# Performance work log

Hardware: AMD Instinct MI355X
Metric: run time of the kernel (lower is better)

## Reference

```python
import jax, jax.numpy as jnp
import numpy as np

HEADS = 3


def layernorm(x, scale, bias):
    mu = x.mean(-1, keepdims=True)
    var = ((x - mu) ** 2).mean(-1, keepdims=True)
    return (x - mu) * jax.lax.rsqrt(var + 1e-5) * scale + bias


def setup_inputs() -> dict:
    key = jax.random.key(0)
    ks = jax.random.split(key, 16)
    B, C, H, W = 8, 64, 32, 32
    hid, out, L = 384, 128, 3
    f32 = jnp.float32
    rn = lambda i, shape, sc: jax.random.normal(ks[i], shape, f32) * sc
    inp = {
        "x": rn(0, (B, C, H, W), 1.0),
        "W_enc": rn(1, (C, hid), 1.0 / np.sqrt(C)),
        "b_enc": jnp.zeros((hid,), f32),
        "gcn_W": rn(2, (L, hid, hid), 1.0 / np.sqrt(hid)),
        "gcn_b": jnp.zeros((L, hid), f32),
        "Wq": rn(3, (L, hid, hid), 1.0 / np.sqrt(hid)),
        "bq": jnp.zeros((L, hid), f32),
        "Wk": rn(4, (L, hid, hid), 1.0 / np.sqrt(hid)),
        "bk": jnp.zeros((L, hid), f32),
        "Wv": rn(5, (L, hid, hid), 1.0 / np.sqrt(hid)),
        "bv": jnp.zeros((L, hid), f32),
        "Wo": rn(6, (L, hid, hid), 1.0 / np.sqrt(hid)),
        "bo": jnp.zeros((L, hid), f32),
        "ln_scale": jnp.ones((L, 3, hid), f32),
        "ln_bias": jnp.zeros((L, 3, hid), f32),
        "mlp_W1": rn(7, (L, hid, 2 * hid), 1.0 / np.sqrt(hid)),
        "mlp_b1": jnp.zeros((L, 2 * hid), f32),
        "mlp_W2": rn(8, (L, 2 * hid, hid), 1.0 / np.sqrt(2 * hid)),
        "mlp_b2": jnp.zeros((L, hid), f32),
        "lin1_W": rn(9, (hid, hid), 1.0 / np.sqrt(hid)),
        "lin1_b": jnp.zeros((hid,), f32),
        "lin2_W": rn(10, (hid, out), 1.0 / np.sqrt(hid)),
        "lin2_b": jnp.zeros((out,), f32),
        "k": 16,
    }
    return inp


def reference(x, W_enc, b_enc, gcn_W, gcn_b, Wq, bq, Wk, bk, Wv, bv, Wo, bo,
              ln_scale, ln_bias, mlp_W1, mlp_b1, mlp_W2, mlp_b2,
              lin1_W, lin1_b, lin2_W, lin2_b, k):
    B, C, H, W = x.shape
    N = H * W
    L = gcn_W.shape[0]

    # node encoder (RWSE expand_x modeled as linear projection of pixel features)
    feats = x.reshape(B, C, N).transpose(0, 2, 1)            # [B, N, C]
    h0 = feats @ W_enc + b_enc                               # [B, N, hid]

    # cosine-similarity graph + kNN hypergraph build
    nh = h0 / jnp.linalg.norm(h0, axis=-1, keepdims=True)
    sim = jnp.einsum('bnd,bmd->bnm', nh, nh)                 # [B, N, N]
    sim = sim - 2.0 * jnp.eye(N, dtype=sim.dtype)            # exclude self-matches
    _, knn_idx = jax.lax.top_k(sim, k)                       # [B, N, k] neighbor (src) ids
    dst = jnp.broadcast_to(jnp.arange(N)[:, None], (N, k)).reshape(-1)  # [N*k]

    def gps_per_graph(hb, src_idx):
        src = src_idx.reshape(-1)                            # [N*k]
        deg = jax.ops.segment_sum(jnp.ones((N * k,), hb.dtype), dst, N) + 1.0  # self-loops
        norm = jax.lax.rsqrt(deg[src] * deg[dst])            # GCN sym norm
        hcur = hb
        for l in range(L):
            # --- local GCN message passing ---
            xw = hcur @ gcn_W[l] + gcn_b[l]                  # [N, hid]
            agg = jax.ops.segment_sum(xw[src] * norm[:, None], dst, N)
            agg = agg + xw / deg[:, None]                    # self-loop term
            h_local = layernorm(hcur + agg, ln_scale[l, 0], ln_bias[l, 0])
            # --- global multihead attention ---
            q = (hcur @ Wq[l] + bq[l]).reshape(N, HEADS, -1)
            kk = (hcur @ Wk[l] + bk[l]).reshape(N, HEADS, -1)
            v = (hcur @ Wv[l] + bv[l]).reshape(N, HEADS, -1)
            dh = q.shape[-1]
            scores = jnp.einsum('nhd,mhd->hnm', q, kk) * (1.0 / np.sqrt(dh))
            attn = jax.nn.softmax(scores, axis=-1)
            o = jnp.einsum('hnm,mhd->nhd', attn, v).reshape(N, -1) @ Wo[l] + bo[l]
            h_attn = layernorm(hcur + o, ln_scale[l, 1], ln_bias[l, 1])
            # --- combine + FFN ---
            out = h_local + h_attn
            out = out + jax.nn.relu(out @ mlp_W1[l] + mlp_b1[l]) @ mlp_W2[l] + mlp_b2[l]
            hcur = layernorm(out, ln_scale[l, 2], ln_bias[l, 2])
        return hcur.mean(axis=0)                             # global mean pool -> [hid]

    pooled = jax.vmap(gps_per_graph)(h0, knn_idx)            # [B, hid]
    z = jax.nn.relu(pooled @ lin1_W + lin1_b)
    return z @ lin2_W + lin2_b                               # [B, out]
```

## Files before the change

kernel.cpp:

```cpp
#include <hip/hip_runtime.h>
#include <hip/hip_bf16.h>

#define B_    8
#define C_    64
#define N_    1024
#define HID   384
#define OUTD  128
#define L_    3
#define KNN   16
#define NHEADS 3
#define DH    128

typedef __attribute__((ext_vector_type(8))) short    s16x8;
typedef __attribute__((ext_vector_type(4))) float    f32x4;
typedef __attribute__((ext_vector_type(8))) unsigned short u16x8;
typedef __attribute__((ext_vector_type(4))) unsigned short u16x4;

__device__ __forceinline__ ushort f2b(float f) {
    uint x = __float_as_uint(f);
    return (ushort)((x + 0x7fff + ((x >> 16) & 1)) >> 16);
}
__device__ __forceinline__ float b2f(uint u) {
    return __uint_as_float(u << 16);
}

__global__ void k_encode(const float* __restrict__ x, const float* __restrict__ Wenc,
                         const float* __restrict__ benc, float* __restrict__ h,
                         float* __restrict__ nh) {
    int bn = blockIdx.x;
    int b = bn >> 10;
    const float* xb = x + (long)b * C_ * N_ + (bn & 1023);
    int tid = threadIdx.x;
    __shared__ float red[128];
    float val[3];
    #pragma unroll
    for (int i = 0; i < 3; ++i) {
        int c0 = tid + i * 128;
        float acc = benc[c0];
        for (int c = 0; c < C_; ++c)
            acc += xb[c * N_] * Wenc[c * HID + c0];
        h[(long)bn * HID + c0] = acc;
        val[i] = acc;
    }
    float ss = 0.f;
    #pragma unroll
    for (int i = 0; i < 3; ++i) ss += val[i] * val[i];
    red[tid] = ss; __syncthreads();
    for (int s = 64; s > 0; s >>= 1) { if (tid < s) red[tid] += red[tid+s]; __syncthreads(); }
    float inv = 1.0f / sqrtf(red[0]);
    #pragma unroll
    for (int i = 0; i < 3; ++i)
        nh[(long)bn * HID + tid + i * 128] = val[i] * inv;
}

template<bool BT, bool RELU>
__global__ __launch_bounds__(256) void k_gemm(
        const float* __restrict__ A, const float* __restrict__ Bm,
        const float* __restrict__ bias, const float* __restrict__ resid,
        float* __restrict__ C, int M, int N, int K,
        long strideA, long strideB, long strideC) {
    __shared__ float As[16][68];
    __shared__ float Bs[16][68];
    int bz = blockIdx.z;
    A  += (long)bz * strideA;
    Bm += (long)bz * strideB;
    C  += (long)bz * strideC;
    int bm = blockIdx.y * 64, bn = blockIdx.x * 64;
    int tid = threadIdx.x;
    int ty = tid >> 4, tx = tid & 15;
    int lm = tid >> 2, lq = tid & 3;
    float acc[4][4] = {};
    for (int k0 = 0; k0 < K; k0 += 16) {
        {
            float4 av = *(const float4*)&A[(long)(bm + lm) * K + k0 + lq * 4];
            As[lq*4+0][lm] = av.x; As[lq*4+1][lm] = av.y;
            As[lq*4+2][lm] = av.z; As[lq*4+3][lm] = av.w;
        }
        if (BT) {
            float4 bv = *(const float4*)&Bm[(long)(bn + lm) * K + k0 + lq * 4];
            Bs[lq*4+0][lm] = bv.x; Bs[lq*4+1][lm] = bv.y;
            Bs[lq*4+2][lm] = bv.z; Bs[lq*4+3][lm] = bv.w;
        } else {
            int kk = tid >> 4, nq = tid & 15;
            float4 bv = *(const float4*)&Bm[(long)(k0 + kk) * N + bn + nq * 4];
            Bs[kk][nq*4+0] = bv.x; Bs[kk][nq*4+1] = bv.y;
            Bs[kk][nq*4+2] = bv.z; Bs[kk][nq*4+3] = bv.w;
        }
        __syncthreads();
        #pragma unroll
        for (int kk = 0; kk < 16; ++kk) {
            float4 a = *(const float4*)&As[kk][ty * 4];
            float4 b = *(const float4*)&Bs[kk][tx * 4];
            acc[0][0] += a.x*b.x; acc[0][1] += a.x*b.y; acc[0][2] += a.x*b.z; acc[0][3] += a.x*b.w;
            acc[1][0] += a.y*b.x; acc[1][1] += a.y*b.y; acc[1][2] += a.y*b.z; acc[1][3] += a.y*b.w;
            acc[2][0] += a.z*b.x; acc[2][1] += a.z*b.y; acc[2][2] += a.z*b.z; acc[2][3] += a.z*b.w;
            acc[3][0] += a.w*b.x; acc[3][1] += a.w*b.y; acc[3][2] += a.w*b.z; acc[3][3] += a.w*b.w;
        }
        __syncthreads();
    }
    #pragma unroll
    for (int i = 0; i < 4; ++i) {
        int row = bm + ty * 4 + i;
        #pragma unroll
        for (int j = 0; j < 4; ++j) {
            int col = bn + tx * 4 + j;
            float c = acc[i][j];
            if (bias)  c += bias[col];
            if (resid) c += resid[(long)row * N + col];
            if (RELU)  c = fmaxf(c, 0.f);
            C[(long)row * N + col] = c;
        }
    }
}

__global__ __launch_bounds__(256) void k_topk(const float* __restrict__ sim, int* __restrict__ knn) {
    int tid = threadIdx.x;
    int wave = tid >> 6, ll = tid & 63;
    int bn = blockIdx.x * 4 + wave;
    int b = bn >> 10, n = bn & 1023;
    const float* row = sim + (long)b * N_ * N_ + (long)n * N_;
    float v[16];
    #pragma unroll
    for (int j = 0; j < 16; ++j) {
        int m = ll + j * 64;
        v[j] = row[m] - (m == n ? 2.0f : 0.0f);
    }
    int* kout = knn + (long)bn * KNN;
    for (int it = 0; it < KNN; ++it) {
        float bv = v[0]; int bi = ll;
        #pragma unroll
        for (int j = 1; j < 16; ++j)
            if (v[j] > bv) { bv = v[j]; bi = ll + j * 64; }
        #pragma unroll
        for (int mask = 1; mask < 64; mask <<= 1) {
            float ov = __shfl_xor(bv, mask);
            int   oi = __shfl_xor(bi, mask);
            if (ov > bv || (ov == bv && oi < bi)) { bv = ov; bi = oi; }
        }
        if (ll == 0) kout[it] = bi;
        if ((bi & 63) == ll) v[bi >> 6] = -1e30f;
    }
}

__global__ void k_cast15(const float* __restrict__ g, const float* __restrict__ q,
                         const float* __restrict__ k, const float* __restrict__ v,
                         const float* __restrict__ o, ushort* __restrict__ out) {
    int z = blockIdx.z; int type = z / 3, l = z % 3;
    const float* in = (type == 0 ? g : type == 1 ? q : type == 2 ? k : type == 3 ? v : o)
                      + (long)l * HID * HID;
    ushort* op = out + (long)z * HID * HID;
    __shared__ float t[32][33];
    int c0 = blockIdx.x * 32, r0 = blockIdx.y * 32;
    int tid = threadIdx.x; int i = tid & 31, j4 = tid >> 5;
    #pragma unroll
    for (int rr = 0; rr < 4; ++rr) {
        int r = j4 * 4 + rr;
        t[r][i] = in[(long)(r0 + r) * HID + c0 + i];
    }
    __syncthreads();
    #pragma unroll
    for (int rr = 0; rr < 4; ++rr) {
        int c = j4 * 4 + rr;
        op[(long)(c0 + c) * HID + r0 + i] = f2b(t[i][c]);
    }
}

__global__ void k_castT(const float* __restrict__ in_, ushort* __restrict__ out_,
                        int R, int C) {
    long mz = (long)blockIdx.z * R * C;
    const float* in = in_ + mz;
    ushort* op = out_ + mz;
    __shared__ float t[32][33];
    int c0 = blockIdx.x * 32, r0 = blockIdx.y * 32;
    int tid = threadIdx.x; int i = tid & 31, j4 = tid >> 5;
    #pragma unroll
    for (int rr = 0; rr < 4; ++rr) {
        int r = j4 * 4 + rr;
        t[r][i] = in[(long)(r0 + r) * C + c0 + i];
    }
    __syncthreads();
    #pragma unroll
    for (int rr = 0; rr < 4; ++rr) {
        int c = j4 * 4 + rr;
        op[(long)(c0 + c) * R + r0 + i] = f2b(t[i][c]);
    }
}

__global__ __launch_bounds__(256) void k_castb(const float* __restrict__ in,
                                               ushort* __restrict__ out) {
    long i0 = ((long)blockIdx.x * 256 + threadIdx.x) * 8;
    float4 a0 = *(const float4*)&in[i0];
    float4 a1 = *(const float4*)&in[i0 + 4];
    u16x8 v;
    v[0]=f2b(a0.x); v[1]=f2b(a0.y); v[2]=f2b(a0.z); v[3]=f2b(a0.w);
    v[4]=f2b(a1.x); v[5]=f2b(a1.y); v[6]=f2b(a1.z); v[7]=f2b(a1.w);
    *(u16x8*)&out[i0] = v;
}

template<int OUTMODE, bool RELU>
__global__ __launch_bounds__(256) void k_mgemm(
        const ushort* __restrict__ A, const ushort* __restrict__ Wt,
        const float* __restrict__ bias, const float* __restrict__ resid,
        void* __restrict__ Cout, int M, int N, int K, long ldcT) {
    __shared__ ushort Al[128][40];
    __shared__ ushort Bl[128][40];
    int bm = blockIdx.y * 128, bnn = blockIdx.x * 128;
    int tid = threadIdx.x;
    int w = tid >> 6, l = tid & 63;
    int wm = w >> 1, wn = w & 1;
    int sr = tid >> 2, skq = (tid & 3) * 8;
    f32x4 acc[4][4] = {};
    for (int k0 = 0; k0 < K; k0 += 32) {
        *(u16x8*)&Al[sr][skq]      = *(const u16x8*)&A [(long)(bm + sr) * K + k0 + skq];
        *(u16x8*)&Al[sr + 64][skq] = *(const u16x8*)&A [(long)(bm + sr + 64) * K + k0 + skq];
        *(u16x8*)&Bl[sr][skq]      = *(const u16x8*)&Wt[(long)(bnn + sr) * K + k0 + skq];
        *(u16x8*)&Bl[sr + 64][skq] = *(const u16x8*)&Wt[(long)(bnn + sr + 64) * K + k0 + skq];
        __syncthreads();
        s16x8 af[4], bf[4];
        #pragma unroll
        for (int mi = 0; mi < 4; ++mi)
            af[mi] = *(const s16x8*)&Al[wm * 64 + mi * 16 + (l & 15)][(l >> 4) * 8];
        #pragma unroll
        for (int ni = 0; ni < 4; ++ni)
            bf[ni] = *(const s16x8*)&Bl[wn * 64 + ni * 16 + (l & 15)][(l >> 4) * 8];
        #pragma unroll
        for (int mi = 0; mi < 4; ++mi)
            #pragma unroll
            for (int ni = 0; ni < 4; ++ni)
                acc[mi][ni] = __builtin_amdgcn_mfma_f32_16x16x32_bf16(af[mi], bf[ni], acc[mi][ni], 0, 0, 0);
        __syncthreads();
    }
    #pragma unroll
    for (int mi = 0; mi < 4; ++mi) {
        int row0 = bm + wm * 64 + mi * 16 + (l >> 4) * 4;
        #pragma unroll
        for (int ni = 0; ni < 4; ++ni) {
            int coln = bnn + wn * 64 + ni * 16 + (l & 15);
            float bv = bias[coln];
            if (OUTMODE == 2) {
                u16x4 pk;
                #pragma unroll
                for (int reg = 0; reg < 4; ++reg)
                    pk[reg] = f2b(acc[mi][ni][reg] + bv);
                *(u16x4*)((ushort*)Cout + (long)coln * ldcT + row0) = pk;
            } else {
                #pragma unroll
                for (int reg = 0; reg < 4; ++reg) {
                    int rowg = row0 + reg;
                    float v = acc[mi][ni][reg] + bv;
                    if (resid) v += resid[(long)rowg * N + coln];
                    if (RELU)  v = fmaxf(v, 0.f);
                    if (OUTMODE == 0) ((float*)Cout)[(long)rowg * N + coln] = v;
                    else              ((ushort*)Cout)[(long)rowg * N + coln] = f2b(v);
                }
            }
        }
    }
}

__global__ void k_gcn_ln(const float* __restrict__ h, const float* __restrict__ xw,
                         const int* __restrict__ knn,
                         const float* __restrict__ lns, const float* __restrict__ lnb,
                         float* __restrict__ hlocal) {
    int bn = blockIdx.x; int b = bn >> 10;
    __shared__ int nb[KNN];
    __shared__ float red[128];
    int tid = threadIdx.x;
    if (tid < KNN) nb[tid] = knn[(long)bn * KNN + tid];
    __syncthreads();
    float val[3]; float sum = 0.f, ssq = 0.f;
    #pragma unroll
    for (int i = 0; i < 3; ++i) {
        int c = tid + i * 128;
        float acc = xw[(long)bn * HID + c];
        #pragma unroll
        for (int j = 0; j < KNN; ++j)
            acc += xw[((long)(b << 10) + nb[j]) * HID + c];
        float v = h[(long)bn * HID + c] + acc * (1.0f / 17.0f);
        val[i] = v; sum += v; ssq += v * v;
    }
    red[tid] = sum; __syncthreads();
    for (int s = 64; s > 0; s >>= 1) { if (tid < s) red[tid] += red[tid+s]; __syncthreads(); }
    sum = red[0]; __syncthreads();
    red[tid] = ssq; __syncthreads();
    for (int s = 64; s > 0; s >>= 1) { if (tid < s) red[tid] += red[tid+s]; __syncthreads(); }
    ssq = red[0];
    float mu = sum / HID;
    float var = ssq / HID - mu * mu;
    float inv = rsqrtf(var + 1e-5f);
    #pragma unroll
    for (int i = 0; i < 3; ++i) {
        int c = tid + i * 128;
        hlocal[(long)bn * HID + c] = (val[i] - mu) * inv * lns[c] + lnb[c];
    }
}

__global__ void k_addln(const float* __restrict__ a, const float* __restrict__ badd,
                        const float* __restrict__ post,
                        const float* __restrict__ lns, const float* __restrict__ lnb,
                        float* __restrict__ outp, ushort* __restrict__ bfout) {
    int bn = blockIdx.x;
    __shared__ float red[128];
    int tid = threadIdx.x;
    float val[3]; float sum = 0.f, ssq = 0.f;
    #pragma unroll
    for (int i = 0; i < 3; ++i) {
        int c = tid + i * 128;
        float v = a[(long)bn * HID + c];
        if (badd) v += badd[(long)bn * HID + c];
        val[i] = v; sum += v; ssq += v * v;
    }
    red[tid] = sum; __syncthreads();
    for (int s = 64; s > 0; s >>= 1) { if (tid < s) red[tid] += red[tid+s]; __syncthreads(); }
    sum = red[0]; __syncthreads();
    red[tid] = ssq; __syncthreads();
    for (int s = 64; s > 0; s >>= 1) { if (tid < s) red[tid] += red[tid+s]; __syncthreads(); }
    ssq = red[0];
    float mu = sum / HID;
    float var = ssq / HID - mu * mu;
    float inv = rsqrtf(var + 1e-5f);
    #pragma unroll
    for (int i = 0; i < 3; ++i) {
        int c = tid + i * 128;
        float o = (val[i] - mu) * inv * lns[c] + lnb[c];
        if (post) o += post[(long)bn * HID + c];
        outp[(long)bn * HID + c] = o;
        if (bfout) bfout[(long)bn * HID + c] = f2b(o);
    }
}

__global__ __launch_bounds__(256) void k_attn(const ushort* __restrict__ qb,
                                              const ushort* __restrict__ kb,
                                              const ushort* __restrict__ vt,
                                              ushort* __restrict__ o) {
    int b = blockIdx.z, hh = blockIdx.y, r0 = blockIdx.x * 16;
    __shared__ ushort sc[16][1032];
    __shared__ ushort kvt[9216];
    __shared__ float rowinv[16];
    int tid = threadIdx.x;
    int w = tid >> 6, l = tid & 63;
    s16x8 aq[4];
    const ushort* qrow = qb + ((long)(b * N_) + r0 + (l & 15)) * HID + hh * DH + (l >> 4) * 8;
    #pragma unroll
    for (int ks = 0; ks < 4; ++ks) aq[ks] = *(const s16x8*)(qrow + ks * 32);
    const float scale = 0.08838834764831845f;
    for (int m0 = 0; m0 < N_; m0 += 64) {
        {
            int key = tid >> 2, seg = tid & 3;
            const ushort* src = kb + ((long)(b * N_) + m0 + key) * HID + hh * DH + seg * 32;
            ushort* dst = &kvt[key * 136 + seg * 32];
            #pragma unroll
            for (int i = 0; i < 4; ++i)
                *(u16x8*)(dst + i * 8) = *(const u16x8*)(src + i * 8);
        }
        __syncthreads();
        f32x4 acc = {0.f, 0.f, 0.f, 0.f};
        #pragma unroll
        for (int ks = 0; ks < 4; ++ks) {
            s16x8 bk = *(const s16x8*)&kvt[(w * 16 + (l & 15)) * 136 + ks * 32 + (l >> 4) * 8];
            acc = __builtin_amdgcn_mfma_f32_16x16x32_bf16(aq[ks], bk, acc, 0, 0, 0);
        }
        int key = m0 + w * 16 + (l & 15);
        #pragma unroll
        for (int reg = 0; reg < 4; ++reg)
            sc[(l >> 4) * 4 + reg][key] = f2b(acc[reg] * scale);
        __syncthreads();
    }
    {
        int g = tid >> 5, l2 = tid & 31;
        #pragma unroll
        for (int rr = 0; rr < 2; ++rr) {
            int row = g + rr * 8;
            float v[32];
            #pragma unroll
            for (int i = 0; i < 16; ++i) {
                uint u = *(const uint*)&sc[row][l2 * 2 + i * 64];
                v[2*i]   = b2f(u & 0xffffu);
                v[2*i+1] = b2f(u >> 16);
            }
            float mx = v[0];
            #pragma unroll
            for (int i = 1; i < 32; ++i) mx = fmaxf(mx, v[i]);
            #pragma unroll
            for (int m = 16; m >= 1; m >>= 1) mx = fmaxf(mx, __shfl_xor(mx, m));
            float sm = 0.f;
            #pragma unroll
            for (int i = 0; i < 16; ++i) {
                float e0 = __expf(v[2*i]   - mx);
                float e1 = __expf(v[2*i+1] - mx);
                sm += e0 + e1;
                *(uint*)&sc[row][l2 * 2 + i * 64] = (uint)f2b(e0) | ((uint)f2b(e1) << 16);
            }
            #pragma unroll
            for (int m = 16; m >= 1; m >>= 1) sm += __shfl_xor(sm, m);
            if (l2 == 0) rowinv[row] = 1.0f / sm;
        }
    }
    __syncthreads();
    f32x4 zero = {0.f, 0.f, 0.f, 0.f};
    f32x4 oacc[2] = {zero, zero};
    for (int m0 = 0; m0 < N_; m0 += 64) {
        {
            int dim = tid >> 1, half = tid & 1;
            const ushort* src = vt + ((long)(hh * DH + dim)) * (B_ * N_) + b * N_ + m0 + half * 32;
            ushort* dst = &kvt[dim * 72 + half * 32];
            #pragma unroll
            for (int i = 0; i < 4; ++i)
                *(u16x8*)(dst + i * 8) = *(const u16x8*)(src + i * 8);
        }
        __syncthreads();
        #pragma unroll
        for (int ks = 0; ks < 2; ++ks) {
            s16x8 pf = *(const s16x8*)&sc[l & 15][m0 + ks * 32 + (l >> 4) * 8];
            #pragma unroll
            for (int d = 0; d < 2; ++d) {
                s16x8 vf = *(const s16x8*)&kvt[((w * 2 + d) * 16 + (l & 15)) * 72 + ks * 32 + (l >> 4) * 8];
                oacc[d] = __builtin_amdgcn_mfma_f32_16x16x32_bf16(pf, vf, oacc[d], 0, 0, 0);
            }
        }
        __syncthreads();
    }
    #pragma unroll
    for (int d = 0; d < 2; ++d) {
        int dim = (w * 2 + d) * 16 + (l & 15);
        #pragma unroll
        for (int reg = 0; reg < 4; ++reg) {
            int row = (l >> 4) * 4 + reg;
            o[((long)(b * N_) + r0 + row) * HID + hh * DH + dim] = f2b(oacc[d][reg] * rowinv[row]);
        }
    }
}

__global__ __launch_bounds__(384) void k_pool1(const float* __restrict__ h,
                                               float* __restrict__ partial) {
    int s = blockIdx.x, b = blockIdx.y;
    int c = threadIdx.x;
    const float* hp = h + ((long)(b * N_) + s * 32) * HID + c;
    float acc = 0.f;
    #pragma unroll
    for (int n = 0; n < 32; ++n) acc += hp[(long)n * HID];
    partial[((long)(b * 32) + s) * HID + c] = acc;
}
__global__ __launch_bounds__(384) void k_pool2(const float* __restrict__ partial,
                                               float* __restrict__ pooled) {
    int b = blockIdx.x;
    int c = threadIdx.x;
    const float* pp = partial + (long)(b * 32) * HID + c;
    float acc = 0.f;
    #pragma unroll
    for (int s = 0; s < 32; ++s) acc += pp[(long)s * HID];
    pooled[b * HID + c] = acc * (1.0f / N_);
}

__global__ void k_head(const float* __restrict__ pooled,
                       const float* __restrict__ w1, const float* __restrict__ b1,
                       const float* __restrict__ w2, const float* __restrict__ b2,
                       float* __restrict__ out) {
    int b = blockIdx.x; int tid = threadIdx.x;
    __shared__ float z[HID];
    float acc = b1[tid];
    for (int c = 0; c < HID; ++c) acc += pooled[b * HID + c] * w1[c * HID + tid];
    z[tid] = fmaxf(acc, 0.f);
    __syncthreads();
    if (tid < OUTD) {
        float a2 = b2[tid];
        for (int j = 0; j < HID; ++j) a2 += z[j] * w2[j * OUTD + tid];
        out[b * OUTD + tid] = a2;
    }
}

extern "C" void kernel_launch(void* const* d_in, const int* in_sizes, int n_in,
                              void* d_out, int out_size, void* d_ws, size_t ws_size,
                              hipStream_t stream) {
    const float* x       = (const float*)d_in[0];
    const float* W_enc   = (const float*)d_in[1];
    const float* b_enc   = (const float*)d_in[2];
    const float* gcn_W   = (const float*)d_in[3];
    const float* gcn_b   = (const float*)d_in[4];
    const float* Wq      = (const float*)d_in[5];
    const float* bq      = (const float*)d_in[6];
    const float* Wk      = (const float*)d_in[7];
    const float* bk      = (const float*)d_in[8];
    const float* Wv      = (const float*)d_in[9];
    const float* bv      = (const float*)d_in[10];
    const float* Wo      = (const float*)d_in[11];
    const float* bo      = (const float*)d_in[12];
    const float* ln_s    = (const float*)d_in[13];
    const float* ln_b    = (const float*)d_in[14];
    const float* mlp_W1  = (const float*)d_in[15];
    const float* mlp_b1  = (const float*)d_in[16];
    const float* mlp_W2  = (const float*)d_in[17];
    const float* mlp_b2  = (const float*)d_in[18];
    const float* lin1_W  = (const float*)d_in[19];
    const float* lin1_b  = (const float*)d_in[20];
    const float* lin2_W  = (const float*)d_in[21];
    const float* lin2_b  = (const float*)d_in[22];

    const long S = (long)B_ * N_ * HID;
    char* base = (char*)d_ws;
    float* h      = (float*)(base);
    float* tmp1   = (float*)(base + (size_t)S * 4);
    float* hlocal = (float*)(base + (size_t)S * 8);
    float* outb   = (float*)(base + (size_t)S * 12);
    char*  tzone  = base + (size_t)S * 16;
    float* proj   = (float*)(base + (size_t)S * 24);
    float*  sim = (float*)tzone;
    ushort* qbf = (ushort*)tzone;
    ushort* kbf = (ushort*)(tzone + (size_t)S * 2);
    ushort* vbT = (ushort*)(tzone + (size_t)S * 4);
    ushort* outb_bf = (ushort*)(tzone + (size_t)S * 6);
    ushort* tb  = (ushort*)tzone;
    int*    knn    = (int*)(base + (size_t)S * 28);
    float*  pooled = (float*)(base + (size_t)S * 28 + 524288);
    ushort* wts    = (ushort*)(base + (size_t)S * 28 + 524288 + 16384);
    const long SQ = (long)HID * HID;
    ushort* w1T = wts + 15 * SQ;
    ushort* w2T = w1T + 3 * (long)HID * 2 * HID;
    ushort* hb  = (ushort*)(base + (size_t)S * 28 + 524288 + 16384 + 7962624);
    float* partial = tmp1;
    ushort* obf = (ushort*)tmp1;

    k_cast15<<<dim3(12, 12, 15), 256, 0, stream>>>(gcn_W, Wq, Wk, Wv, Wo, wts);
    k_castT<<<dim3(24, 12, 3), 256, 0, stream>>>(mlp_W1, w1T, HID, 2 * HID);
    k_castT<<<dim3(12, 24, 3), 256, 0, stream>>>(mlp_W2, w2T, 2 * HID, HID);

    k_encode<<<B_ * N_, 128, 0, stream>>>(x, W_enc, b_enc, h, tmp1);
    k_gemm<true, false><<<dim3(16, 16, B_), 256, 0, stream>>>(
        tmp1, tmp1, nullptr, nullptr, sim, N_, N_, HID,
        (long)N_ * HID, (long)N_ * HID, (long)N_ * N_);
    k_topk<<<B_ * N_ / 4, 256, 0, stream>>>(sim, knn);
    k_castb<<<(int)(S / 2048), 256, 0, stream>>>(h, hb);

    const int M = B_ * N_;
    for (int l = 0; l < L_; ++l) {
        const ushort* gWt = wts + (long)(0 + l) * SQ;
        const ushort* wqT = wts + (long)(3 + l) * SQ;
        const ushort* wkT = wts + (long)(6 + l) * SQ;
        const ushort* wvT = wts + (long)(9 + l) * SQ;
        const ushort* woT = wts + (long)(12 + l) * SQ;
        const ushort* w1Tl = w1T + (long)l * HID * 2 * HID;
        const ushort* w2Tl = w2T + (long)l * HID * 2 * HID;
        const float* gB  = gcn_b + (long)l * HID;
        const float* bql = bq + (long)l * HID;
        const float* bkl = bk + (long)l * HID;
        const float* bvl = bv + (long)l * HID;
        const float* bol = bo + (long)l * HID;
        const float* b1l = mlp_b1 + (long)l * 2 * HID;
        const float* b2l = mlp_b2 + (long)l * HID;
        const float* ls0 = ln_s + (long)(l * 3 + 0) * HID; const float* lb0 = ln_b + (long)(l * 3 + 0) * HID;
        const float* ls1 = ln_s + (long)(l * 3 + 1) * HID; const float* lb1 = ln_b + (long)(l * 3 + 1) * HID;
        const float* ls2 = ln_s + (long)(l * 3 + 2) * HID; const float* lb2 = ln_b + (long)(l * 3 + 2) * HID;

        k_mgemm<0, false><<<dim3(HID / 128, M / 128), 256, 0, stream>>>(
            hb, gWt, gB, nullptr, tmp1, M, HID, HID, 0);
        k_gcn_ln<<<B_ * N_, 128, 0, stream>>>(h, tmp1, knn, ls0, lb0, hlocal);
        k_mgemm<1, false><<<dim3(HID / 128, M / 128), 256, 0, stream>>>(
            hb, wqT, bql, nullptr, qbf, M, HID, HID, 0);
        k_mgemm<1, false><<<dim3(HID / 128, M / 128), 256, 0, stream>>>(
            hb, wkT, bkl, nullptr, kbf, M, HID, HID, 0);
        k_mgemm<2, false><<<dim3(HID / 128, M / 128), 256, 0, stream>>>(
            hb, wvT, bvl, nullptr, vbT, M, HID, HID, (long)M);
        k_attn<<<dim3(N_ / 16, NHEADS, B_), 256, 0, stream>>>(qbf, kbf, vbT, obf);
        k_mgemm<0, false><<<dim3(HID / 128, M / 128), 256, 0, stream>>>(
            obf, woT, bol, nullptr, proj, M, HID, HID, 0);
        k_addln<<<B_ * N_, 128, 0, stream>>>(h, proj, hlocal, ls1, lb1, outb, outb_bf);
        k_mgemm<1, true><<<dim3(2 * HID / 128, M / 128), 256, 0, stream>>>(
            outb_bf, w1Tl, b1l, nullptr, tb, M, 2 * HID, HID, 0);
        k_mgemm<0, false><<<dim3(HID / 128, M / 128), 256, 0, stream>>>(
            tb, w2Tl, b2l, outb, tmp1, M, HID, 2 * HID, 0);
        k_addln<<<B_ * N_, 128, 0, stream>>>(tmp1, nullptr, nullptr, ls2, lb2, h, hb);
    }

    k_pool1<<<dim3(32, B_), 384, 0, stream>>>(h, partial);
    k_pool2<<<B_, 384, 0, stream>>>(partial, pooled);
    k_head<<<B_, HID, 0, stream>>>(pooled, lin1_W, lin1_b, lin2_W, lin2_b,
                                   (float*)d_out);
}
```

Baseline: 996.8 us.

## Use split-bf16 MFMA for similarity GEMM and fuse QKV projections

Measured after the change: 875.0 us. 1.14x faster.

```diff
diff --git a/kernel.cpp b/kernel.cpp
--- a/kernel.cpp
+++ b/kernel.cpp
@@ -26,7 +26,8 @@
 
 __global__ void k_encode(const float* __restrict__ x, const float* __restrict__ Wenc,
                          const float* __restrict__ benc, float* __restrict__ h,
-                         float* __restrict__ nh) {
+                         ushort* __restrict__ hb,
+                         ushort* __restrict__ nhh, ushort* __restrict__ nhl) {
     int bn = blockIdx.x;
     int b = bn >> 10;
     const float* xb = x + (long)b * C_ * N_ + (bn & 1023);
@@ -40,6 +41,7 @@
         for (int c = 0; c < C_; ++c)
             acc += xb[c * N_] * Wenc[c * HID + c0];
         h[(long)bn * HID + c0] = acc;
+        hb[(long)bn * HID + c0] = f2b(acc);
         val[i] = acc;
     }
     float ss = 0.f;
@@ -49,66 +51,70 @@
     for (int s = 64; s > 0; s >>= 1) { if (tid < s) red[tid] += red[tid+s]; __syncthreads(); }
     float inv = 1.0f / sqrtf(red[0]);
     #pragma unroll
-    for (int i = 0; i < 3; ++i)
-        nh[(long)bn * HID + tid + i * 128] = val[i] * inv;
-}
-
-template<bool BT, bool RELU>
-__global__ __launch_bounds__(256) void k_gemm(
-        const float* __restrict__ A, const float* __restrict__ Bm,
-        const float* __restrict__ bias, const float* __restrict__ resid,
-        float* __restrict__ C, int M, int N, int K,
-        long strideA, long strideB, long strideC) {
-    __shared__ float As[16][68];
-    __shared__ float Bs[16][68];
+    for (int i = 0; i < 3; ++i) {
+        int c0 = tid + i * 128;
+        float fv = val[i] * inv;
+        ushort hu = f2b(fv);
+        float lo = fv - b2f((uint)hu);
+        nhh[(long)bn * HID + c0] = hu;
+        nhl[(long)bn * HID + c0] = f2b(lo);
+    }
+}
+
+__global__ __launch_bounds__(256) void k_sim(const ushort* __restrict__ nhh,
+                                             const ushort* __restrict__ nhl,
+                                             float* __restrict__ sim) {
+    __shared__ ushort Ah[128][40], Alo[128][40], Bh[128][40], Blo[128][40];
     int bz = blockIdx.z;
-    A  += (long)bz * strideA;
-    Bm += (long)bz * strideB;
-    C  += (long)bz * strideC;
-    int bm = blockIdx.y * 64, bn = blockIdx.x * 64;
-    int tid = threadIdx.x;
-    int ty = tid >> 4, tx = tid & 15;
-    int lm = tid >> 2, lq = tid & 3;
-    float acc[4][4] = {};
-    for (int k0 = 0; k0 < K; k0 += 16) {
-        {
-            float4 av = *(const float4*)&A[(long)(bm + lm) * K + k0 + lq * 4];
-            As[lq*4+0][lm] = av.x; As[lq*4+1][lm] = av.y;
-            As[lq*4+2][lm] = av.z; As[lq*4+3][lm] = av.w;
-        }
-        if (BT) {
-            float4 bv = *(const float4*)&Bm[(long)(bn + lm) * K + k0 + lq * 4];
-            Bs[lq*4+0][lm] = bv.x; Bs[lq*4+1][lm] = bv.y;
-            Bs[lq*4+2][lm] = bv.z; Bs[lq*4+3][lm] = bv.w;
-        } else {
-            int kk = tid >> 4, nq = tid & 15;
-            float4 bv = *(const float4*)&Bm[(long)(k0 + kk) * N + bn + nq * 4];
-            Bs[kk][nq*4+0] = bv.x; Bs[kk][nq*4+1] = bv.y;
-            Bs[kk][nq*4+2] = bv.z; Bs[kk][nq*4+3] = bv.w;
-        }
-        __syncthreads();
-        #pragma unroll
-        for (int kk = 0; kk < 16; ++kk) {
-            float4 a = *(const float4*)&As[kk][ty * 4];
-            float4 b = *(const float4*)&Bs[kk][tx * 4];
-            acc[0][0] += a.x*b.x; acc[0][1] += a.x*b.y; acc[0][2] += a.x*b.z; acc[0][3] += a.x*b.w;
-            acc[1][0] += a.y*b.x; acc[1][1] += a.y*b.y; acc[1][2] += a.y*b.z; acc[1][3] += a.y*b.w;
-            acc[2][0] += a.z*b.x; acc[2][1] += a.z*b.y; acc[2][2] += a.z*b.z; acc[2][3] += a.z*b.w;
-            acc[3][0] += a.w*b.x; acc[3][1] += a.w*b.y; acc[3][2] += a.w*b.z; acc[3][3] += a.w*b.w;
-        }
-        __syncthreads();
-    }
-    #pragma unroll
-    for (int i = 0; i < 4; ++i) {
-        int row = bm + ty * 4 + i;
-        #pragma unroll
-        for (int j = 0; j < 4; ++j) {
-            int col = bn + tx * 4 + j;
-            float c = acc[i][j];
-            if (bias)  c += bias[col];
-            if (resid) c += resid[(long)row * N + col];
-            if (RELU)  c = fmaxf(c, 0.f);
-            C[(long)row * N + col] = c;
+    int bm = blockIdx.y * 128, bn = blockIdx.x * 128;
+    const ushort* baseh = nhh + (long)bz * N_ * HID;
+    const ushort* basel = nhl + (long)bz * N_ * HID;
+    int tid = threadIdx.x;
+    int w = tid >> 6, l = tid & 63;
+    int wm = w >> 1, wn = w & 1;
+    int sr = tid >> 2, skq = (tid & 3) * 8;
+    f32x4 acc[4][4] = {};
+    for (int k0 = 0; k0 < HID; k0 += 32) {
+        *(u16x8*)&Ah [sr][skq]      = *(const u16x8*)&baseh[(long)(bm + sr) * HID + k0 + skq];
+        *(u16x8*)&Ah [sr + 64][skq] = *(const u16x8*)&baseh[(long)(bm + sr + 64) * HID + k0 + skq];
+        *(u16x8*)&Alo[sr][skq]      = *(const u16x8*)&basel[(long)(bm + sr) * HID + k0 + skq];
+        *(u16x8*)&Alo[sr + 64][skq] = *(const u16x8*)&basel[(long)(bm + sr + 64) * HID + k0 + skq];
+        *(u16x8*)&Bh [sr][skq]      = *(const u16x8*)&baseh[(long)(bn + sr) * HID + k0 + skq];
+        *(u16x8*)&Bh [sr + 64][skq] = *(const u16x8*)&baseh[(long)(bn + sr + 64) * HID + k0 + skq];
+        *(u16x8*)&Blo[sr][skq]      = *(const u16x8*)&basel[(long)(bn + sr) * HID + k0 + skq];
+        *(u16x8*)&Blo[sr + 64][skq] = *(const u16x8*)&basel[(long)(bn + sr + 64) * HID + k0 + skq];
+        __syncthreads();
+        s16x8 ah[4], al[4], bh[4], bl[4];
+        #pragma unroll
+        for (int mi = 0; mi < 4; ++mi) {
+            ah[mi] = *(const s16x8*)&Ah [wm * 64 + mi * 16 + (l & 15)][(l >> 4) * 8];
+            al[mi] = *(const s16x8*)&Alo[wm * 64 + mi * 16 + (l & 15)][(l >> 4) * 8];
+        }
+        #pragma unroll
+        for (int ni = 0; ni < 4; ++ni) {
+            bh[ni] = *(const s16x8*)&Bh [wn * 64 + ni * 16 + (l & 15)][(l >> 4) * 8];
+            bl[ni] = *(const s16x8*)&Blo[wn * 64 + ni * 16 + (l & 15)][(l >> 4) * 8];
+        }
+        #pragma unroll
+        for (int mi = 0; mi < 4; ++mi)
+            #pragma unroll
+            for (int ni = 0; ni < 4; ++ni) {
+                acc[mi][ni] = __builtin_amdgcn_mfma_f32_16x16x32_bf16(ah[mi], bh[ni], acc[mi][ni], 0, 0, 0);
+                acc[mi][ni] = __builtin_amdgcn_mfma_f32_16x16x32_bf16(ah[mi], bl[ni], acc[mi][ni], 0, 0, 0);
+                acc[mi][ni] = __builtin_amdgcn_mfma_f32_16x16x32_bf16(al[mi], bh[ni], acc[mi][ni], 0, 0, 0);
+            }
+        __syncthreads();
+    }
+    float* so = sim + (long)bz * N_ * N_;
+    #pragma unroll
+    for (int mi = 0; mi < 4; ++mi) {
+        int row0 = bm + wm * 64 + mi * 16 + (l >> 4) * 4;
+        #pragma unroll
+        for (int ni = 0; ni < 4; ++ni) {
+            int coln = bn + wn * 64 + ni * 16 + (l & 15);
+            #pragma unroll
+            for (int reg = 0; reg < 4; ++reg)
+                so[(long)(row0 + reg) * N_ + coln] = acc[mi][ni][reg];
         }
     }
 }
@@ -148,7 +154,8 @@
     int z = blockIdx.z; int type = z / 3, l = z % 3;
     const float* in = (type == 0 ? g : type == 1 ? q : type == 2 ? k : type == 3 ? v : o)
                       + (long)l * HID * HID;
-    ushort* op = out + (long)z * HID * HID;
+    int slot = (type == 0) ? l : (type == 4) ? 12 + l : 3 + l * 3 + (type - 1);
+    ushort* op = out + (long)slot * HID * HID;
     __shared__ float t[32][33];
     int c0 = blockIdx.x * 32, r0 = blockIdx.y * 32;
     int tid = threadIdx.x; int i = tid & 31, j4 = tid >> 5;
@@ -186,22 +193,20 @@
     }
 }
 
-__global__ __launch_bounds__(256) void k_castb(const float* __restrict__ in,
-                                               ushort* __restrict__ out) {
-    long i0 = ((long)blockIdx.x * 256 + threadIdx.x) * 8;
-    float4 a0 = *(const float4*)&in[i0];
-    float4 a1 = *(const float4*)&in[i0 + 4];
-    u16x8 v;
-    v[0]=f2b(a0.x); v[1]=f2b(a0.y); v[2]=f2b(a0.z); v[3]=f2b(a0.w);
-    v[4]=f2b(a1.x); v[5]=f2b(a1.y); v[6]=f2b(a1.z); v[7]=f2b(a1.w);
-    *(u16x8*)&out[i0] = v;
+__global__ void k_biasqkv(const float* __restrict__ bq, const float* __restrict__ bk,
+                          const float* __restrict__ bv, float* __restrict__ qkvb) {
+    int l = blockIdx.x, t = threadIdx.x;
+    qkvb[l * 1152 + t]       = bq[l * HID + t];
+    qkvb[l * 1152 + 384 + t] = bk[l * HID + t];
+    qkvb[l * 1152 + 768 + t] = bv[l * HID + t];
 }
 
 template<int OUTMODE, bool RELU>
 __global__ __launch_bounds__(256) void k_mgemm(
         const ushort* __restrict__ A, const ushort* __restrict__ Wt,
         const float* __restrict__ bias, const float* __restrict__ resid,
-        void* __restrict__ Cout, int M, int N, int K, long ldcT) {
+        void* __restrict__ Cout, void* __restrict__ CoutT,
+        int M, int N, int K, long ldcT) {
     __shared__ ushort Al[128][40];
     __shared__ ushort Bl[128][40];
     int bm = blockIdx.y * 128, bnn = blockIdx.x * 128;
@@ -243,6 +248,18 @@
                 for (int reg = 0; reg < 4; ++reg)
                     pk[reg] = f2b(acc[mi][ni][reg] + bv);
                 *(u16x4*)((ushort*)Cout + (long)coln * ldcT + row0) = pk;
+            } else if (OUTMODE == 3) {
+                if (coln < 768) {
+                    #pragma unroll
+                    for (int reg = 0; reg < 4; ++reg)
+                        ((ushort*)Cout)[(long)(row0 + reg) * 768 + coln] = f2b(acc[mi][ni][reg] + bv);
+                } else {
+                    u16x4 pk;
+                    #pragma unroll
+                    for (int reg = 0; reg < 4; ++reg)
+                        pk[reg] = f2b(acc[mi][ni][reg] + bv);
+                    *(u16x4*)((ushort*)CoutT + (long)(coln - 768) * ldcT + row0) = pk;
+                }
             } else {
                 #pragma unroll
                 for (int reg = 0; reg < 4; ++reg) {
@@ -329,8 +346,7 @@
     }
 }
 
-__global__ __launch_bounds__(256) void k_attn(const ushort* __restrict__ qb,
-                                              const ushort* __restrict__ kb,
+__global__ __launch_bounds__(256) void k_attn(const ushort* __restrict__ qk,
                                               const ushort* __restrict__ vt,
                                               ushort* __restrict__ o) {
     int b = blockIdx.z, hh = blockIdx.y, r0 = blockIdx.x * 16;
@@ -340,14 +356,14 @@
     int tid = threadIdx.x;
     int w = tid >> 6, l = tid & 63;
     s16x8 aq[4];
-    const ushort* qrow = qb + ((long)(b * N_) + r0 + (l & 15)) * HID + hh * DH + (l >> 4) * 8;
+    const ushort* qrow = qk + ((long)(b * N_) + r0 + (l & 15)) * 768 + hh * DH + (l >> 4) * 8;
     #pragma unroll
     for (int ks = 0; ks < 4; ++ks) aq[ks] = *(const s16x8*)(qrow + ks * 32);
     const float scale = 0.08838834764831845f;
     for (int m0 = 0; m0 < N_; m0 += 64) {
         {
             int key = tid >> 2, seg = tid & 3;
-            const ushort* src = kb + ((long)(b * N_) + m0 + key) * HID + hh * DH + seg * 32;
+            const ushort* src = qk + ((long)(b * N_) + m0 + key) * 768 + 384 + hh * DH + seg * 32;
             ushort* dst = &kvt[key * 136 + seg * 32];
             #pragma unroll
             for (int i = 0; i < 4; ++i)
@@ -505,11 +521,12 @@
     char*  tzone  = base + (size_t)S * 16;
     float* proj   = (float*)(base + (size_t)S * 24);
     float*  sim = (float*)tzone;
-    ushort* qbf = (ushort*)tzone;
-    ushort* kbf = (ushort*)(tzone + (size_t)S * 2);
-    ushort* vbT = (ushort*)(tzone + (size_t)S * 4);
+    ushort* qkbf = (ushort*)tzone;
+    ushort* vbT  = (ushort*)(tzone + (size_t)S * 4);
     ushort* outb_bf = (ushort*)(tzone + (size_t)S * 6);
     ushort* tb  = (ushort*)tzone;
+    ushort* nhh = (ushort*)(base + (size_t)S * 4);
+    ushort* nhl = (ushort*)(base + (size_t)S * 6);
     int*    knn    = (int*)(base + (size_t)S * 28);
     float*  pooled = (float*)(base + (size_t)S * 28 + 524288);
     ushort* wts    = (ushort*)(base + (size_t)S * 28 + 524288 + 16384);
@@ -517,33 +534,27 @@
     ushort* w1T = wts + 15 * SQ;
     ushort* w2T = w1T + 3 * (long)HID * 2 * HID;
     ushort* hb  = (ushort*)(base + (size_t)S * 28 + 524288 + 16384 + 7962624);
+    float* qkvb = (float*)(base + (size_t)S * 28 + 524288 + 16384 + 7962624 + (size_t)S * 2);
     float* partial = tmp1;
     ushort* obf = (ushort*)tmp1;
 
     k_cast15<<<dim3(12, 12, 15), 256, 0, stream>>>(gcn_W, Wq, Wk, Wv, Wo, wts);
     k_castT<<<dim3(24, 12, 3), 256, 0, stream>>>(mlp_W1, w1T, HID, 2 * HID);
     k_castT<<<dim3(12, 24, 3), 256, 0, stream>>>(mlp_W2, w2T, 2 * HID, HID);
-
-    k_encode<<<B_ * N_, 128, 0, stream>>>(x, W_enc, b_enc, h, tmp1);
-    k_gemm<true, false><<<dim3(16, 16, B_), 256, 0, stream>>>(
-        tmp1, tmp1, nullptr, nullptr, sim, N_, N_, HID,
-        (long)N_ * HID, (long)N_ * HID, (long)N_ * N_);
+    k_biasqkv<<<3, 384, 0, stream>>>(bq, bk, bv, qkvb);
+
+    k_encode<<<B_ * N_, 128, 0, stream>>>(x, W_enc, b_enc, h, hb, nhh, nhl);
+    k_sim<<<dim3(8, 8, 8), 256, 0, stream>>>(nhh, nhl, sim);
     k_topk<<<B_ * N_ / 4, 256, 0, stream>>>(sim, knn);
-    k_castb<<<(int)(S / 2048), 256, 0, stream>>>(h, hb);
 
     const int M = B_ * N_;
     for (int l = 0; l < L_; ++l) {
-        const ushort* gWt = wts + (long)(0 + l) * SQ;
-        const ushort* wqT = wts + (long)(3 + l) * SQ;
-        const ushort* wkT = wts + (long)(6 + l) * SQ;
-        const ushort* wvT = wts + (long)(9 + l) * SQ;
-        const ushort* woT = wts + (long)(12 + l) * SQ;
+        const ushort* gWt  = wts + (long)l * SQ;
+        const ushort* qkvW = wts + (long)(3 + l * 3) * SQ;
+        const ushort* woT  = wts + (long)(12 + l) * SQ;
         const ushort* w1Tl = w1T + (long)l * HID * 2 * HID;
         const ushort* w2Tl = w2T + (long)l * HID * 2 * HID;
         const float* gB  = gcn_b + (long)l * HID;
-        const float* bql = bq + (long)l * HID;
-        const float* bkl = bk + (long)l * HID;
-        const float* bvl = bv + (long)l * HID;
         const float* bol = bo + (long)l * HID;
         const float* b1l = mlp_b1 + (long)l * 2 * HID;
         const float* b2l = mlp_b2 + (long)l * HID;
@@ -552,22 +563,18 @@
         const float* ls2 = ln_s + (long)(l * 3 + 2) * HID; const float* lb2 = ln_b + (long)(l * 3 + 2) * HID;
 
         k_mgemm<0, false><<<dim3(HID / 128, M / 128), 256, 0, stream>>>(
-            hb, gWt, gB, nullptr, tmp1, M, HID, HID, 0);
+            hb, gWt, gB, nullptr, tmp1, nullptr, M, HID, HID, 0);
         k_gcn_ln<<<B_ * N_, 128, 0, stream>>>(h, tmp1, knn, ls0, lb0, hlocal);
-        k_mgemm<1, false><<<dim3(HID / 128, M / 128), 256, 0, stream>>>(
-            hb, wqT, bql, nullptr, qbf, M, HID, HID, 0);
-        k_mgemm<1, false><<<dim3(HID / 128, M / 128), 256, 0, stream>>>(
-            hb, wkT, bkl, nullptr, kbf, M, HID, HID, 0);
-        k_mgemm<2, false><<<dim3(HID / 128, M / 128), 256, 0, stream>>>(
-            hb, wvT, bvl, nullptr, vbT, M, HID, HID, (long)M);
-        k_attn<<<dim3(N_ / 16, NHEADS, B_), 256, 0, stream>>>(qbf, kbf, vbT, obf);
+        k_mgemm<3, false><<<dim3(1152 / 128, M / 128), 256, 0, stream>>>(
+            hb, qkvW, qkvb + l * 1152, nullptr, qkbf, vbT, M, 1152, HID, (long)M);
+        k_attn<<<dim3(N_ / 16, NHEADS, B_), 256, 0, stream>>>(qkbf, vbT, obf);
         k_mgemm<0, false><<<dim3(HID / 128, M / 128), 256, 0, stream>>>(
-            obf, woT, bol, nullptr, proj, M, HID, HID, 0);
+            obf, woT, bol, nullptr, proj, nullptr, M, HID, HID, 0);
         k_addln<<<B_ * N_, 128, 0, stream>>>(h, proj, hlocal, ls1, lb1, outb, outb_bf);
         k_mgemm<1, true><<<dim3(2 * HID / 128, M / 128), 256, 0, stream>>>(
-            outb_bf, w1Tl, b1l, nullptr, tb, M, 2 * HID, HID, 0);
+            outb_bf, w1Tl, b1l, nullptr, tb, nullptr, M, 2 * HID, HID, 0);
         k_mgemm<0, false><<<dim3(HID / 128, M / 128), 256, 0, stream>>>(
-            tb, w2Tl, b2l, outb, tmp1, M, HID, 2 * HID, 0);
+            tb, w2Tl, b2l, outb, tmp1, nullptr, M, HID, 2 * HID, 0);
         k_addln<<<B_ * N_, 128, 0, stream>>>(tmp1, nullptr, nullptr, ls2, lb2, h, hb);
     }
 
```
